# Optimization experiments

Hardware: AMD Instinct MI355X
Metric: run time of the kernel (lower is better)

The kernel has to match this reference:

```python
import jax, jax.numpy as jnp
import numpy as np

N, E = 25000, 400000
D_NODE, D_EDGE_IN, D_EH, D_H, D_DUAL = 128, 16, 128, 256, 128


def layer_norm(x, g, b, eps=1e-5):
    mu = jnp.mean(x, axis=-1, keepdims=True)
    var = jnp.mean((x - mu) ** 2, axis=-1, keepdims=True)
    return (x - mu) * jax.lax.rsqrt(var + eps) * g + b


def setup_inputs() -> dict:
    key = jax.random.key(0)
    ks = jax.random.split(key, 20)

    def w(k, shape):
        return (jax.random.normal(k, shape, dtype=jnp.float32) * 0.05)

    inp = {
        "node_embedding": jax.random.normal(ks[0], (N, D_NODE), dtype=jnp.float32),
        "edge_index": jax.random.randint(ks[1], (2, E), 0, N, dtype=jnp.int64),
        "edge_attr": jax.random.normal(ks[2], (E, D_EDGE_IN), dtype=jnp.float32),
        "dual_node_emb": jax.random.normal(ks[3], (E, D_DUAL), dtype=jnp.float32),
        "atom_reactivity_logits": jax.random.normal(ks[4], (N,), dtype=jnp.float32),
        "W_be1": w(ks[5], (D_EDGE_IN, D_EH)), "b_be1": jnp.zeros((D_EH,), jnp.float32),
        "g_be1": jnp.ones((D_EH,), jnp.float32), "bb_be1": jnp.zeros((D_EH,), jnp.float32),
        "W_be2": w(ks[6], (D_EH, D_EH)), "b_be2": jnp.zeros((D_EH,), jnp.float32),
        "g_be2": jnp.ones((D_EH,), jnp.float32), "bb_be2": jnp.zeros((D_EH,), jnp.float32),
        "W_be3": w(ks[7], (D_EH, D_EH)), "b_be3": jnp.zeros((D_EH,), jnp.float32),
        "g_be3": jnp.ones((D_EH,), jnp.float32), "bb_be3": jnp.zeros((D_EH,), jnp.float32),
        # DualGraphBondReactivityPredictor
        "W_d1": w(ks[8], (D_DUAL, D_H)), "b_d1": jnp.zeros((D_H,), jnp.float32),
        "W_d2": w(ks[9], (D_H, D_H)), "b_d2": jnp.zeros((D_H,), jnp.float32),
        "W_do": w(ks[10], (D_H, 1)), "b_do": jnp.zeros((1,), jnp.float32),
        # main head: in = 2*D_NODE + D_EH + 3 = 387
        "W_f1": w(ks[11], (2 * D_NODE + D_EH + 3, D_H)), "b_f1": jnp.zeros((D_H,), jnp.float32),
        "W_f2": w(ks[12], (D_H, D_H)), "b_f2": jnp.zeros((D_H,), jnp.float32),
        "W_bo": w(ks[13], (D_H, 1)), "b_bo": jnp.zeros((1,), jnp.float32),
    }
    return inp


def reference(node_embedding, edge_index, edge_attr, dual_node_emb, atom_reactivity_logits,
              W_be1, b_be1, g_be1, bb_be1, W_be2, b_be2, g_be2, bb_be2,
              W_be3, b_be3, g_be3, bb_be3,
              W_d1, b_d1, W_d2, b_d2, W_do, b_do,
              W_f1, b_f1, W_f2, b_f2, W_bo, b_bo):
    src, dst = edge_index[0], edge_index[1]

    # BondEmbedding (dropout = identity in eval mode)
    e = jax.nn.silu(layer_norm(edge_attr @ W_be1 + b_be1, g_be1, bb_be1))
    e = jax.nn.silu(layer_norm(e @ W_be2 + b_be2, g_be2, bb_be2))
    e = jax.nn.silu(layer_norm(e @ W_be3 + b_be3, g_be3, bb_be3))  # [E, D_EH]

    atom_p = jax.nn.sigmoid(atom_reactivity_logits)  # [N]
    p_src = atom_p[src][:, None]  # [E,1]
    p_dst = atom_p[dst][:, None]

    # dual-graph bond reactivity
    d = jax.nn.silu(dual_node_emb @ W_d1 + b_d1)
    d = jax.nn.silu(d @ W_d2 + b_d2)
    dual_p = jax.nn.sigmoid((d @ W_do + b_do)[:, 0])[:, None]  # [E,1]

    feats = jnp.concatenate(
        [node_embedding[src], node_embedding[dst], e, dual_p, p_src, p_dst], axis=-1
    )  # [E, 2*D_NODE + D_EH + 3]

    x = jax.nn.silu(feats @ W_f1 + b_f1)
    x = jax.nn.silu(x @ W_f2 + b_f2)
    return (x @ W_bo + b_bo)[:, 0]  # [E]
```

## Files before the change

kernel.cpp:

```cpp
#include <hip/hip_runtime.h>
#include <hip/hip_bf16.h>
#include <stdint.h>

typedef __attribute__((ext_vector_type(8))) short bf16x8;
typedef __attribute__((ext_vector_type(4))) float f32x4;
typedef __attribute__((ext_vector_type(4))) float float4v;

__device__ __forceinline__ uint16_t bfc(float x){
    __hip_bfloat16 h = __float2bfloat16(x);
    return __builtin_bit_cast(uint16_t, h);
}
__device__ __forceinline__ uint32_t pk2(float a, float b){
    return (uint32_t)bfc(a) | ((uint32_t)bfc(b) << 16);
}
__device__ __forceinline__ float fsigmoid(float x){ return 1.0f / (1.0f + __expf(-x)); }
__device__ __forceinline__ float fsilu(float x){ return x * fsigmoid(x); }

__device__ __forceinline__ bf16x8 pack8(float4v lo, float4v hi){
    bf16x8 r;
    r[0]=(short)bfc(lo[0]); r[1]=(short)bfc(lo[1]);
    r[2]=(short)bfc(lo[2]); r[3]=(short)bfc(lo[3]);
    r[4]=(short)bfc(hi[0]); r[5]=(short)bfc(hi[1]);
    r[6]=(short)bfc(hi[2]); r[7]=(short)bfc(hi[3]);
    return r;
}

#define SZ_BE1 4096
#define SZ_128 16384
#define SZ_D1  32768
#define SZ_D2  65536
#define SZ_F1  98304
#define OFF_BE1 0
#define OFF_BE2 (OFF_BE1 + SZ_BE1)
#define OFF_BE3 (OFF_BE2 + SZ_128)
#define OFF_D1  (OFF_BE3 + SZ_128)
#define OFF_D2  (OFF_D1 + SZ_D1)
#define OFF_F1  (OFF_D2 + SZ_D2)
#define OFF_F2  (OFF_F1 + SZ_F1)
#define WS_ELEMS (OFF_F2 + SZ_D2)

__device__ __forceinline__ int fragpos(int k, int c, int OUT){
    int kt = k >> 5, ct = c >> 4;
    int fid = kt * (OUT >> 4) + ct;
    int ln = ((k & 31) >> 3) * 16 + (c & 15);
    return fid * 512 + ln * 8 + (k & 7);
}

__global__ void __launch_bounds__(256)
prep_w(const float* __restrict__ Wbe1, const float* __restrict__ Wbe2,
       const float* __restrict__ Wbe3, const float* __restrict__ Wd1,
       const float* __restrict__ Wd2,  const float* __restrict__ Wf1,
       const float* __restrict__ Wf2,  uint16_t* __restrict__ ws){
    int t = blockIdx.x * 256 + threadIdx.x;
    if (t >= WS_ELEMS) return;
    if (t < OFF_BE2) {
        int u = t;            int k = u >> 7, c = u & 127;
        float v = (k < 16) ? Wbe1[k * 128 + c] : 0.0f;
        ws[OFF_BE1 + fragpos(k, c, 128)] = bfc(v);
    } else if (t < OFF_BE3) {
        int u = t - OFF_BE2;  int k = u >> 7, c = u & 127;
        ws[OFF_BE2 + fragpos(k, c, 128)] = bfc(Wbe2[u]);
    } else if (t < OFF_D1) {
        int u = t - OFF_BE3;  int k = u >> 7, c = u & 127;
        ws[OFF_BE3 + fragpos(k, c, 128)] = bfc(Wbe3[u]);
    } else if (t < OFF_D2) {
        int u = t - OFF_D1;   int k = u >> 8, c = u & 255;
        ws[OFF_D1 + fragpos(k, c, 256)] = bfc(Wd1[u]);
    } else if (t < OFF_F1) {
        int u = t - OFF_D2;   int k = u >> 8, c = u & 255;
        ws[OFF_D2 + fragpos(k, c, 256)] = bfc(Wd2[u]);
    } else if (t < OFF_F2) {
        int u = t - OFF_F1;   int k = u >> 8, c = u & 255;
        ws[OFF_F1 + fragpos(k, c, 256)] = bfc(Wf1[u]);
    } else {
        int u = t - OFF_F2;   int k = u >> 8, c = u & 255;
        ws[OFF_F2 + fragpos(k, c, 256)] = bfc(Wf2[u]);
    }
}

__global__ void __launch_bounds__(256)
prep_n(const float* __restrict__ src, uint16_t* __restrict__ dst, int n){
    int t = blockIdx.x * 256 + threadIdx.x;
    if (t < n) dst[t] = bfc(src[t]);
}

typedef const __attribute__((address_space(1))) void gas_void;
typedef __attribute__((address_space(3))) void las_void;
__device__ __forceinline__ void g2l16(const void* g, void* l){
    __builtin_amdgcn_global_load_lds((gas_void*)g, (las_void*)l, 16, 0, 0);
}

#define LDS_TOTAL 135168

__global__ void __launch_bounds__(512) __attribute__((amdgpu_waves_per_eu(2, 2)))
bond_fast_kernel(const int* __restrict__ edge_index,
                 const float* __restrict__ edge_attr, const float* __restrict__ dual_emb,
                 const float* __restrict__ logits,
                 const float* __restrict__ b_be1, const float* __restrict__ g_be1, const float* __restrict__ bb_be1,
                 const float* __restrict__ b_be2, const float* __restrict__ g_be2, const float* __restrict__ bb_be2,
                 const float* __restrict__ b_be3, const float* __restrict__ g_be3, const float* __restrict__ bb_be3,
                 const float* __restrict__ b_d1, const float* __restrict__ b_d2,
                 const float* __restrict__ W_do, const float* __restrict__ b_do,
                 const float* __restrict__ W_f1, const float* __restrict__ b_f1,
                 const float* __restrict__ b_f2,
                 const float* __restrict__ W_bo, const float* __restrict__ b_bo,
                 const uint16_t* __restrict__ ws, float* __restrict__ out, int E)
{
    __shared__ char lds[LDS_TOTAL];
    const int t    = threadIdx.x;
    const int wave = t >> 6;
    const int lane = t & 63;
    const int li   = lane & 15, lg = lane >> 4;
    const int eg   = wave >> 1;
    const int ch   = wave & 1;
    const int e0b  = blockIdx.x * 128;

    char* bufE = lds;
    char* h256 = lds + 32768;
    uint16_t* wb0 = (uint16_t*)(lds + 98304);
    uint16_t* wb1 = (uint16_t*)(lds + 114688);
    float* ps  = (float*)(lds + 131072);
    float* pd  = (float*)(lds + 131584);
    int* sidx  = (int*)(lds + 132096);
    int* didx  = (int*)(lds + 132608);
    float* dpp = (float*)(lds + 133120);
    float* bop = (float*)(lds + 134144);

    const uint8_t*  wsb = (const uint8_t*)ws;
    const uint16_t* nbf = ws + WS_ELEMS;

    if (t < 128) {
        int e = e0b + t; if (e >= E) e = E - 1;
        int s_ = edge_index[e];
        int d_ = edge_index[E + e];
        sidx[t] = s_; didx[t] = d_;
        ps[t] = fsigmoid(logits[s_]);
        pd[t] = fsigmoid(logits[d_]);
    }

    int cur = 0;
    auto stageW = [&](int elemoff, int big){
        uint8_t* dst = (uint8_t*)(cur ? wb0 : wb1) + t * 16;
        const uint8_t* g = wsb + (size_t)elemoff * 2 + t * 16;
        g2l16(g, dst);
        if (big) g2l16(g + 8192, dst + 8192);
    };
    auto stepend = [&](){ __syncthreads(); cur ^= 1; };
    auto curbuf  = [&]() -> const uint16_t* { return cur ? wb1 : wb0; };

    f32x4 acc[2][8];

    auto ldf = [&](const uint16_t* w, int fid) -> bf16x8 {
        return *(const bf16x8*)(w + fid * 512 + lane * 8);
    };
    auto grpBE = [&](const uint16_t* w, bf16x8 a0){
        #pragma unroll
        for (int ct = 0; ct < 8; ++ct){
            bf16x8 b = ldf(w, ct);
            acc[0][ct] = __builtin_amdgcn_mfma_f32_16x16x32_bf16(a0, b, acc[0][ct], 0, 0, 0);
        }
    };
    auto grp256 = [&](const uint16_t* w, bf16x8 a0, bf16x8 a1){
        #pragma unroll
        for (int ct = 0; ct < 8; ++ct){
            bf16x8 b = ldf(w, ch * 8 + ct);
            acc[0][ct] = __builtin_amdgcn_mfma_f32_16x16x32_bf16(a0, b, acc[0][ct], 0, 0, 0);
            acc[1][ct] = __builtin_amdgcn_mfma_f32_16x16x32_bf16(a1, b, acc[1][ct], 0, 0, 0);
        }
    };
    auto initBE = [&](const float* b){
        #pragma unroll
        for (int ct = 0; ct < 8; ++ct){
            float bv = b[li + 16 * ct];
            f32x4 iv = {bv, bv, bv, bv};
            acc[0][ct] = iv;
        }
    };
    auto init256 = [&](const float* b){
        #pragma unroll
        for (int ct = 0; ct < 8; ++ct){
            float bv = b[ch * 128 + ct * 16 + li];
            f32x4 iv = {bv, bv, bv, bv};
            acc[0][ct] = iv; acc[1][ct] = iv;
        }
    };
    auto eb_read = [&](int row, int kt) -> bf16x8 {
        int off = row * 256 + (kt * 32 + lg * 8) * 2;
        return *(const bf16x8*)(bufE + (off ^ ((row & 7) << 4)));
    };
    auto h2_read = [&](int row, int kt) -> bf16x8 {
        int off = row * 512 + (kt * 32 + lg * 8) * 2;
        return *(const bf16x8*)(h256 + (off ^ ((row & 7) << 4)));
    };
    auto lnstoreBE = [&](const float* g, const float* bb){
        #pragma unroll
        for (int r = 0; r < 4; ++r){
            float s = 0.f, q = 0.f;
            #pragma unroll
            for (int ct = 0; ct < 8; ++ct){ float v = acc[0][ct][r]; s += v; q += v*v; }
            s += __shfl_xor(s, 1); q += __shfl_xor(q, 1);
            s += __shfl_xor(s, 2); q += __shfl_xor(q, 2);
            s += __shfl_xor(s, 4); q += __shfl_xor(q, 4);
            s += __shfl_xor(s, 8); q += __shfl_xor(q, 8);
            float mu = s * 0.0078125f;
            float var = q * 0.0078125f - mu * mu;
            float rs = rsqrtf(var + 1e-5f);
            int row = wave * 16 + lg * 4 + r;
            int rswz = (row & 7) << 4;
            #pragma unroll
            for (int ct = 0; ct < 8; ++ct){
                int col = li + 16 * ct;
                float v = (acc[0][ct][r] - mu) * rs * g[col] + bb[col];
                int off = row * 256 + col * 2;
                *(uint16_t*)(bufE + (off ^ rswz)) = bfc(fsilu(v));
            }
        }
    };
    auto silustore256 = [&](){
        #pragma unroll
        for (int rt = 0; rt < 2; ++rt){
            #pragma unroll
            for (int r = 0; r < 4; ++r){
                int row = eg * 32 + rt * 16 + lg * 4 + r;
                int rswz = (row & 7) << 4;
                #pragma unroll
                for (int ct = 0; ct < 8; ++ct){
                    int off = row * 512 + (ch * 128 + ct * 16 + li) * 2;
                    *(uint16_t*)(h256 + (off ^ rswz)) = bfc(fsilu(acc[rt][ct][r]));
                }
            }
        }
    };

    {
        const uint8_t* g = wsb + t * 16;
        g2l16(g, (uint8_t*)wb0 + t * 16);
    }
    __syncthreads();

    {
        stageW(OFF_BE2, 0);
        bf16x8 aE = {0,0,0,0,0,0,0,0};
        if (lg < 2){
            int ea = e0b + wave * 16 + li; if (ea >= E) ea = E - 1;
            const float* pa = edge_attr + (size_t)ea * 16 + lg * 8;
            aE = pack8(*(const float4v*)pa, *(const float4v*)(pa + 4));
        }
        initBE(b_be1);
        grpBE(curbuf(), aE);
        lnstoreBE(g_be1, bb_be1);
        stepend();
    }

    initBE(b_be2);
    #pragma unroll 1
    for (int kt = 0; kt < 4; ++kt){
        if (kt < 3) stageW(OFF_BE2 + (kt + 1) * 4096, 0);
        else        stageW(OFF_BE3, 0);
        grpBE(curbuf(), eb_read(wave * 16 + li, kt));
        if (kt == 3) lnstoreBE(g_be2, bb_be2);
        stepend();
    }
    initBE(b_be3);
    #pragma unroll 1
    for (int kt = 0; kt < 4; ++kt){
        if (kt < 3) stageW(OFF_BE3 + (kt + 1) * 4096, 0);
        else        stageW(OFF_D1, 1);
        grpBE(curbuf(), eb_read(wave * 16 + li, kt));
        if (kt == 3) lnstoreBE(g_be3, bb_be3);
        stepend();
    }

    init256(b_d1);
    #pragma unroll 1
    for (int kt = 0; kt < 4; ++kt){
        float4v va0, va1, vb0, vb1;
        {
            int ea = e0b + eg * 32 + li;      if (ea >= E) ea = E - 1;
            int eb = e0b + eg * 32 + 16 + li; if (eb >= E) eb = E - 1;
            const float* pa = dual_emb + (size_t)ea * 128 + kt * 32 + lg * 8;
            const float* pb = dual_emb + (size_t)eb * 128 + kt * 32 + lg * 8;
            va0 = *(const float4v*)pa; va1 = *(const float4v*)(pa + 4);
            vb0 = *(const float4v*)pb; vb1 = *(const float4v*)(pb + 4);
        }
        if (kt < 3) stageW(OFF_D1 + (kt + 1) * 8192, 1);
        else        stageW(OFF_D2, 1);
        grp256(curbuf(), pack8(va0, va1), pack8(vb0, vb1));
        if (kt == 3) silustore256();
        stepend();
    }

    init256(b_d2);
    #pragma unroll 1
    for (int kt = 0; kt < 8; ++kt){
        if (kt < 7) stageW(OFF_D2 + (kt + 1) * 8192, 1);
        else        stageW(OFF_F1, 1);
        grp256(curbuf(), h2_read(eg * 32 + li, kt), h2_read(eg * 32 + 16 + li, kt));
        if (kt == 7){
            #pragma unroll
            for (int rt = 0; rt < 2; ++rt){
                #pragma unroll
                for (int r = 0; r < 4; ++r){
                    float s = 0.f;
                    #pragma unroll
                    for (int ct = 0; ct < 8; ++ct)
                        s += fsilu(acc[rt][ct][r]) * W_do[ch * 128 + ct * 16 + li];
                    s += __shfl_xor(s, 1); s += __shfl_xor(s, 2);
                    s += __shfl_xor(s, 4); s += __shfl_xor(s, 8);
                    if (li == 0) dpp[ch * 128 + eg * 32 + rt * 16 + lg * 4 + r] = s;
                }
            }
        }
        stepend();
    }

    {
        {
            float bdo0 = b_do[0];
            #pragma unroll
            for (int ct = 0; ct < 8; ++ct){
                int col = ch * 128 + ct * 16 + li;
                float bv = b_f1[col];
                float t0 = W_f1[384 * 256 + col];
                float t1 = W_f1[385 * 256 + col];
                float t2 = W_f1[386 * 256 + col];
                #pragma unroll
                for (int rt = 0; rt < 2; ++rt)
                    #pragma unroll
                    for (int r = 0; r < 4; ++r){
                        int row = eg * 32 + rt * 16 + lg * 4 + r;
                        float dv = fsigmoid(dpp[row] + dpp[128 + row] + bdo0);
                        acc[rt][ct][r] = bv + dv*t0 + ps[row]*t1 + pd[row]*t2;
                    }
            }
        }
        int s0 = sidx[eg * 32 + li],      s1 = sidx[eg * 32 + 16 + li];
        int d0 = didx[eg * 32 + li],      d1 = didx[eg * 32 + 16 + li];
        #pragma unroll 1
        for (int kt = 0; kt < 12; ++kt){
            bf16x8 a0, a1;
            if (kt < 8){
                int ra = (kt < 4) ? s0 : d0;
                int rb = (kt < 4) ? s1 : d1;
                int ko = (kt & 3) * 32 + lg * 8;
                a0 = *(const bf16x8*)(nbf + (size_t)ra * 128 + ko);
                a1 = *(const bf16x8*)(nbf + (size_t)rb * 128 + ko);
            } else {
                a0 = eb_read(eg * 32 + li, kt - 8);
                a1 = eb_read(eg * 32 + 16 + li, kt - 8);
            }
            if (kt < 11) stageW(OFF_F1 + (kt + 1) * 8192, 1);
            else         stageW(OFF_F2, 1);
            grp256(curbuf(), a0, a1);
            if (kt == 11) silustore256();
            stepend();
        }
    }

    init256(b_f2);
    #pragma unroll 1
    for (int kt = 0; kt < 8; ++kt){
        if (kt < 7) stageW(OFF_F2 + (kt + 1) * 8192, 1);
        grp256(curbuf(), h2_read(eg * 32 + li, kt), h2_read(eg * 32 + 16 + li, kt));
        if (kt == 7){
            #pragma unroll
            for (int rt = 0; rt < 2; ++rt){
                #pragma unroll
                for (int r = 0; r < 4; ++r){
                    float s = 0.f;
                    #pragma unroll
                    for (int ct = 0; ct < 8; ++ct)
                        s += fsilu(acc[rt][ct][r]) * W_bo[ch * 128 + ct * 16 + li];
                    s += __shfl_xor(s, 1); s += __shfl_xor(s, 2);
                    s += __shfl_xor(s, 4); s += __shfl_xor(s, 8);
                    if (li == 0) bop[ch * 128 + eg * 32 + rt * 16 + lg * 4 + r] = s;
                }
            }
        } else {
            stepend();
        }
    }
    __syncthreads();
    if (t < 128){
        int e = e0b + t;
        if (e < E) out[e] = bop[t] + bop[128 + t] + b_bo[0];
    }
}

__global__ void __launch_bounds__(512) __attribute__((amdgpu_waves_per_eu(2, 2)))
bond_fused_kernel(const float* __restrict__ node_emb, const int* __restrict__ edge_index,
                  const float* __restrict__ edge_attr, const float* __restrict__ dual_emb,
                  const float* __restrict__ logits,
                  const float* __restrict__ W_be1, const float* __restrict__ b_be1,
                  const float* __restrict__ g_be1, const float* __restrict__ bb_be1,
                  const float* __restrict__ W_be2, const float* __restrict__ b_be2,
                  const float* __restrict__ g_be2, const float* __restrict__ bb_be2,
                  const float* __restrict__ W_be3, const float* __restrict__ b_be3,
                  const float* __restrict__ g_be3, const float* __restrict__ bb_be3,
                  const float* __restrict__ W_d1, const float* __restrict__ b_d1,
                  const float* __restrict__ W_d2, const float* __restrict__ b_d2,
                  const float* __restrict__ W_do, const float* __restrict__ b_do,
                  const float* __restrict__ W_f1, const float* __restrict__ b_f1,
                  const float* __restrict__ W_f2, const float* __restrict__ b_f2,
                  const float* __restrict__ W_bo, const float* __restrict__ b_bo,
                  float* __restrict__ out, int E)
{
    __shared__ char lds[LDS_TOTAL];
    const int t    = threadIdx.x;
    const int wave = t >> 6;
    const int lane = t & 63;
    const int li   = lane & 15, lg = lane >> 4;
    const int eg   = wave >> 1;
    const int ch   = wave & 1;
    const int e0b  = blockIdx.x * 128;

    char* bufE = lds;
    char* h256 = lds + 32768;
    uint16_t* wb0 = (uint16_t*)(lds + 98304);
    uint16_t* wb1 = (uint16_t*)(lds + 114688);
    float* ps  = (float*)(lds + 131072);
    float* pd  = (float*)(lds + 131584);
    int* sidx  = (int*)(lds + 132096);
    int* didx  = (int*)(lds + 132608);
    float* dpp = (float*)(lds + 133120);
    float* bop = (float*)(lds + 134144);

    if (t < 128) {
        int e = e0b + t; if (e >= E) e = E - 1;
        int s_ = edge_index[e];
        int d_ = edge_index[E + e];
        sidx[t] = s_; didx[t] = d_;
        ps[t] = fsigmoid(logits[s_]);
        pd[t] = fsigmoid(logits[d_]);
    }

    float sr[2][8];
    auto issueW256 = [&](const float* W, int kbase){
        #pragma unroll
        for (int h = 0; h < 2; ++h){
            const float* p = W + (size_t)(kbase + lg * 8) * 256 + (wave + 8*h) * 16 + li;
            #pragma unroll
            for (int j = 0; j < 8; ++j) sr[h][j] = p[j * 256];
        }
    };
    auto issueW128 = [&](const float* W, int kbase, int K){
        const float* p = W + (size_t)(kbase + lg * 8) * 128 + wave * 16 + li;
        #pragma unroll
        for (int j = 0; j < 8; ++j)
            sr[0][j] = (kbase + lg * 8 + j < K) ? p[j * 128] : 0.f;
    };
    auto commitW = [&](uint16_t* dst, int nh){
        #pragma unroll
        for (int h = 0; h < 2; ++h){
            if (h < nh){
                uint4 w;
                w.x = pk2(sr[h][0], sr[h][1]); w.y = pk2(sr[h][2], sr[h][3]);
                w.z = pk2(sr[h][4], sr[h][5]); w.w = pk2(sr[h][6], sr[h][7]);
                *(uint4*)(dst + (wave + 8*h) * 512 + lane * 8) = w;
            }
        }
    };

    int cur = 0;
    auto stepend = [&](int mode){
        if (mode) commitW(cur ? wb0 : wb1, mode == 128 ? 1 : 2);
        __syncthreads();
        cur ^= 1;
    };
    auto curbuf = [&]() -> const uint16_t* { return cur ? wb1 : wb0; };

    f32x4 acc[2][8];

    auto ldf = [&](const uint16_t* w, int fid) -> bf16x8 {
        return *(const bf16x8*)(w + fid * 512 + lane * 8);
    };
    auto grpBE = [&](const uint16_t* w, bf16x8 a0){
        #pragma unroll
        for (int ct = 0; ct < 8; ++ct){
            bf16x8 b = ldf(w, ct);
            acc[0][ct] = __builtin_amdgcn_mfma_f32_16x16x32_bf16(a0, b, acc[0][ct], 0, 0, 0);
        }
    };
    auto grp256 = [&](const uint16_t* w, bf16x8 a0, bf16x8 a1){
        #pragma unroll
        for (int ct = 0; ct < 8; ++ct){
            bf16x8 b = ldf(w, ch * 8 + ct);
            acc[0][ct] = __builtin_amdgcn_mfma_f32_16x16x32_bf16(a0, b, acc[0][ct], 0, 0, 0);
            acc[1][ct] = __builtin_amdgcn_mfma_f32_16x16x32_bf16(a1, b, acc[1][ct], 0, 0, 0);
        }
    };
    auto initBE = [&](const float* b){
        #pragma unroll
        for (int ct = 0; ct < 8; ++ct){
            float bv = b[li + 16 * ct];
            f32x4 iv = {bv, bv, bv, bv};
            acc[0][ct] = iv;
        }
    };
    auto init256 = [&](const float* b){
        #pragma unroll
        for (int ct = 0; ct < 8; ++ct){
            float bv = b[ch * 128 + ct * 16 + li];
            f32x4 iv = {bv, bv, bv, bv};
            acc[0][ct] = iv; acc[1][ct] = iv;
        }
    };
    auto eb_read = [&](int row, int kt) -> bf16x8 {
        int off = row * 256 + (kt * 32 + lg * 8) * 2;
        return *(const bf16x8*)(bufE + (off ^ ((row & 7) << 4)));
    };
    auto h2_read = [&](int row, int kt) -> bf16x8 {
        int off = row * 512 + (kt * 32 + lg * 8) * 2;
        return *(const bf16x8*)(h256 + (off ^ ((row & 7) << 4)));
    };
    auto lnstoreBE = [&](const float* g, const float* bb){
        #pragma unroll
        for (int r = 0; r < 4; ++r){
            float s = 0.f, q = 0.f;
            #pragma unroll
            for (int ct = 0; ct < 8; ++ct){ float v = acc[0][ct][r]; s += v; q += v*v; }
            s += __shfl_xor(s, 1); q += __shfl_xor(q, 1);
            s += __shfl_xor(s, 2); q += __shfl_xor(q, 2);
            s += __shfl_xor(s, 4); q += __shfl_xor(q, 4);
            s += __shfl_xor(s, 8); q += __shfl_xor(q, 8);
            float mu = s * 0.0078125f;
            float var = q * 0.0078125f - mu * mu;
            float rs = rsqrtf(var + 1e-5f);
            int row = wave * 16 + lg * 4 + r;
            int rswz = (row & 7) << 4;
            #pragma unroll
            for (int ct = 0; ct < 8; ++ct){
                int col = li + 16 * ct;
                float v = (acc[0][ct][r] - mu) * rs * g[col] + bb[col];
                int off = row * 256 + col * 2;
                *(uint16_t*)(bufE + (off ^ rswz)) = bfc(fsilu(v));
            }
        }
    };
    auto silustore256 = [&](){
        #pragma unroll
        for (int rt = 0; rt < 2; ++rt){
            #pragma unroll
            for (int r = 0; r < 4; ++r){
                int row = eg * 32 + rt * 16 + lg * 4 + r;
                int rswz = (row & 7) << 4;
                #pragma unroll
                for (int ct = 0; ct < 8; ++ct){
                    int off = row * 512 + (ch * 128 + ct * 16 + li) * 2;
                    *(uint16_t*)(h256 + (off ^ rswz)) = bfc(fsilu(acc[rt][ct][r]));
                }
            }
        }
    };

    issueW128(W_be1, 0, 16);
    commitW(wb0, 1);
    __syncthreads();

    {
        bf16x8 aE = {0,0,0,0,0,0,0,0};
        if (lg < 2){
            int ea = e0b + wave * 16 + li; if (ea >= E) ea = E - 1;
            const float* pa = edge_attr + (size_t)ea * 16 + lg * 8;
            aE = pack8(*(const float4v*)pa, *(const float4v*)(pa + 4));
        }
        issueW128(W_be2, 0, 128);
        initBE(b_be1);
        grpBE(curbuf(), aE);
        lnstoreBE(g_be1, bb_be1);
        stepend(128);
    }

    initBE(b_be2);
    #pragma unroll 1
    for (int kt = 0; kt < 4; ++kt){
        if (kt < 3) issueW128(W_be2, (kt + 1) * 32, 128);
        else        issueW128(W_be3, 0, 128);
        grpBE(curbuf(), eb_read(wave * 16 + li, kt));
        if (kt == 3) lnstoreBE(g_be2, bb_be2);
        stepend(128);
    }
    initBE(b_be3);
    #pragma unroll 1
    for (int kt = 0; kt < 4; ++kt){
        if (kt < 3) issueW128(W_be3, (kt + 1) * 32, 128);
        else        issueW256(W_d1, 0);
        grpBE(curbuf(), eb_read(wave * 16 + li, kt));
        if (kt == 3) lnstoreBE(g_be3, bb_be3);
        stepend(kt < 3 ? 128 : 256);
    }

    init256(b_d1);
    #pragma unroll 1
    for (int kt = 0; kt < 4; ++kt){
        float4v va0, va1, vb0, vb1;
        {
            int ea = e0b + eg * 32 + li;      if (ea >= E) ea = E - 1;
            int eb = e0b + eg * 32 + 16 + li; if (eb >= E) eb = E - 1;
            const float* pa = dual_emb + (size_t)ea * 128 + kt * 32 + lg * 8;
            const float* pb = dual_emb + (size_t)eb * 128 + kt * 32 + lg * 8;
            va0 = *(const float4v*)pa; va1 = *(const float4v*)(pa + 4);
            vb0 = *(const float4v*)pb; vb1 = *(const float4v*)(pb + 4);
        }
        if (kt < 3) issueW256(W_d1, (kt + 1) * 32);
        else        issueW256(W_d2, 0);
        grp256(curbuf(), pack8(va0, va1), pack8(vb0, vb1));
        if (kt == 3) silustore256();
        stepend(256);
    }

    init256(b_d2);
    #pragma unroll 1
    for (int kt = 0; kt < 8; ++kt){
        if (kt < 7) issueW256(W_d2, (kt + 1) * 32);
        else        issueW256(W_f1, 0);
        grp256(curbuf(), h2_read(eg * 32 + li, kt), h2_read(eg * 32 + 16 + li, kt));
        if (kt == 7){
            #pragma unroll
            for (int rt = 0; rt < 2; ++rt){
                #pragma unroll
                for (int r = 0; r < 4; ++r){
                    float s = 0.f;
                    #pragma unroll
                    for (int ct = 0; ct < 8; ++ct)
                        s += fsilu(acc[rt][ct][r]) * W_do[ch * 128 + ct * 16 + li];
                    s += __shfl_xor(s, 1); s += __shfl_xor(s, 2);
                    s += __shfl_xor(s, 4); s += __shfl_xor(s, 8);
                    if (li == 0) dpp[ch * 128 + eg * 32 + rt * 16 + lg * 4 + r] = s;
                }
            }
        }
        stepend(256);
    }

    {
        {
            float bdo0 = b_do[0];
            #pragma unroll
            for (int ct = 0; ct < 8; ++ct){
                int col = ch * 128 + ct * 16 + li;
                float bv = b_f1[col];
                float t0 = W_f1[384 * 256 + col];
                float t1 = W_f1[385 * 256 + col];
                float t2 = W_f1[386 * 256 + col];
                #pragma unroll
                for (int rt = 0; rt < 2; ++rt)
                    #pragma unroll
                    for (int r = 0; r < 4; ++r){
                        int row = eg * 32 + rt * 16 + lg * 4 + r;
                        float dv = fsigmoid(dpp[row] + dpp[128 + row] + bdo0);
                        acc[rt][ct][r] = bv + dv*t0 + ps[row]*t1 + pd[row]*t2;
                    }
            }
        }
        int s0 = sidx[eg * 32 + li],      s1 = sidx[eg * 32 + 16 + li];
        int d0 = didx[eg * 32 + li],      d1 = didx[eg * 32 + 16 + li];
        #pragma unroll 1
        for (int kt = 0; kt < 12; ++kt){
            bf16x8 a0, a1;
            if (kt < 8){
                int ra = (kt < 4) ? s0 : d0;
                int rb = (kt < 4) ? s1 : d1;
                int ko = (kt & 3) * 32 + lg * 8;
                const float* pa = node_emb + (size_t)ra * 128 + ko;
                const float* pb = node_emb + (size_t)rb * 128 + ko;
                a0 = pack8(*(const float4v*)pa, *(const float4v*)(pa + 4));
                a1 = pack8(*(const float4v*)pb, *(const float4v*)(pb + 4));
            } else {
                a0 = eb_read(eg * 32 + li, kt - 8);
                a1 = eb_read(eg * 32 + 16 + li, kt - 8);
            }
            if (kt < 11) issueW256(W_f1, (kt + 1) * 32);
            else         issueW256(W_f2, 0);
            grp256(curbuf(), a0, a1);
            if (kt == 11) silustore256();
            stepend(256);
        }
    }

    init256(b_f2);
    #pragma unroll 1
    for (int kt = 0; kt < 8; ++kt){
        if (kt < 7) issueW256(W_f2, (kt + 1) * 32);
        grp256(curbuf(), h2_read(eg * 32 + li, kt), h2_read(eg * 32 + 16 + li, kt));
        if (kt == 7){
            #pragma unroll
            for (int rt = 0; rt < 2; ++rt){
                #pragma unroll
                for (int r = 0; r < 4; ++r){
                    float s = 0.f;
                    #pragma unroll
                    for (int ct = 0; ct < 8; ++ct)
                        s += fsilu(acc[rt][ct][r]) * W_bo[ch * 128 + ct * 16 + li];
                    s += __shfl_xor(s, 1); s += __shfl_xor(s, 2);
                    s += __shfl_xor(s, 4); s += __shfl_xor(s, 8);
                    if (li == 0) bop[ch * 128 + eg * 32 + rt * 16 + lg * 4 + r] = s;
                }
            }
        } else {
            stepend(256);
        }
    }
    __syncthreads();
    if (t < 128){
        int e = e0b + t;
        if (e < E) out[e] = bop[t] + bop[128 + t] + b_bo[0];
    }
}

extern "C" void kernel_launch(void* const* d_in, const int* in_sizes, int n_in,
                              void* d_out, int out_size, void* d_ws, size_t ws_size,
                              hipStream_t stream) {
    const float* node_emb   = (const float*)d_in[0];
    const int*   edge_index = (const int*)d_in[1];
    const float* edge_attr  = (const float*)d_in[2];
    const float* dual_emb   = (const float*)d_in[3];
    const float* logits     = (const float*)d_in[4];
    const float* W_be1 = (const float*)d_in[5];
    const float* b_be1 = (const float*)d_in[6];
    const float* g_be1 = (const float*)d_in[7];
    const float* bb_be1= (const float*)d_in[8];
    const float* W_be2 = (const float*)d_in[9];
    const float* b_be2 = (const float*)d_in[10];
    const float* g_be2 = (const float*)d_in[11];
    const float* bb_be2= (const float*)d_in[12];
    const float* W_be3 = (const float*)d_in[13];
    const float* b_be3 = (const float*)d_in[14];
    const float* g_be3 = (const float*)d_in[15];
    const float* bb_be3= (const float*)d_in[16];
    const float* W_d1  = (const float*)d_in[17];
    const float* b_d1  = (const float*)d_in[18];
    const float* W_d2  = (const float*)d_in[19];
    const float* b_d2  = (const float*)d_in[20];
    const float* W_do  = (const float*)d_in[21];
    const float* b_do  = (const float*)d_in[22];
    const float* W_f1  = (const float*)d_in[23];
    const float* b_f1  = (const float*)d_in[24];
    const float* W_f2  = (const float*)d_in[25];
    const float* b_f2  = (const float*)d_in[26];
    const float* W_bo  = (const float*)d_in[27];
    const float* b_bo  = (const float*)d_in[28];
    float* out = (float*)d_out;

    int E = in_sizes[2] / 16;
    int nblocks = (E + 127) / 128;
    size_t nodeElems = (size_t)in_sizes[0];
    size_t wsNeed = ((size_t)WS_ELEMS + nodeElems) * 2;

    if (ws_size >= wsNeed) {
        uint16_t* ws16 = (uint16_t*)d_ws;
        prep_w<<<dim3((WS_ELEMS + 255) / 256), dim3(256), 0, stream>>>(
            W_be1, W_be2, W_be3, W_d1, W_d2, W_f1, W_f2, ws16);
        prep_n<<<dim3((int)((nodeElems + 255) / 256)), dim3(256), 0, stream>>>(
            node_emb, ws16 + WS_ELEMS, (int)nodeElems);
        bond_fast_kernel<<<dim3(nblocks), dim3(512), 0, stream>>>(
            edge_index, edge_attr, dual_emb, logits,
            b_be1, g_be1, bb_be1,
            b_be2, g_be2, bb_be2,
            b_be3, g_be3, bb_be3,
            b_d1, b_d2, W_do, b_do,
            W_f1, b_f1, b_f2, W_bo, b_bo,
            ws16, out, E);
    } else {
        bond_fused_kernel<<<dim3(nblocks), dim3(512), 0, stream>>>(
            node_emb, edge_index, edge_attr, dual_emb, logits,
            W_be1, b_be1, g_be1, bb_be1,
            W_be2, b_be2, g_be2, bb_be2,
            W_be3, b_be3, g_be3, bb_be3,
            W_d1, b_d1, W_d2, b_d2, W_do, b_do,
            W_f1, b_f1, W_f2, b_f2, W_bo, b_bo,
            out, E);
    }
}
```

Measured before the change: 774.2 us.

## Double workgroup to 1024 threads, one 16-row tile per wave

The fast kernel now launches 1024 threads per 128-edge block instead of 512. Each wave handles a single 16-row M tile instead of two, so the accumulator array halves and register pressure drops. Weight staging is rebalanced: the upper 512 threads stage the 8 KB BondEmbedding slices while the lower 8 waves compute that stage, leaving half the waves idle during it. The goal is more waves in flight to hide latency, but each weight fragment read from LDS is now reused across only one A tile, which doubles LDS traffic per MFMA and adds more barrier participants.

New measurement: 805.5 us. 1.04x slower.

```diff
diff --git a/kernel.cpp b/kernel.cpp
--- a/kernel.cpp
+++ b/kernel.cpp
@@ -92,7 +92,7 @@
 
 #define LDS_TOTAL 135168
 
-__global__ void __launch_bounds__(512) __attribute__((amdgpu_waves_per_eu(2, 2)))
+__global__ void __launch_bounds__(1024) __attribute__((amdgpu_waves_per_eu(4, 4)))
 bond_fast_kernel(const int* __restrict__ edge_index,
                  const float* __restrict__ edge_attr, const float* __restrict__ dual_emb,
                  const float* __restrict__ logits,
@@ -139,16 +139,21 @@
     }
 
     int cur = 0;
-    auto stageW = [&](int elemoff, int big){
+    auto stageW16 = [&](int elemoff){
         uint8_t* dst = (uint8_t*)(cur ? wb0 : wb1) + t * 16;
-        const uint8_t* g = wsb + (size_t)elemoff * 2 + t * 16;
-        g2l16(g, dst);
-        if (big) g2l16(g + 8192, dst + 8192);
+        g2l16(wsb + (size_t)elemoff * 2 + t * 16, dst);
+    };
+    auto stageW8 = [&](int elemoff){
+        if (t >= 512){
+            int u = t - 512;
+            uint8_t* dst = (uint8_t*)(cur ? wb0 : wb1) + u * 16;
+            g2l16(wsb + (size_t)elemoff * 2 + u * 16, dst);
+        }
     };
     auto stepend = [&](){ __syncthreads(); cur ^= 1; };
     auto curbuf  = [&]() -> const uint16_t* { return cur ? wb1 : wb0; };
 
-    f32x4 acc[2][8];
+    f32x4 acc[8];
 
     auto ldf = [&](const uint16_t* w, int fid) -> bf16x8 {
         return *(const bf16x8*)(w + fid * 512 + lane * 8);
@@ -157,15 +162,14 @@
         #pragma unroll
         for (int ct = 0; ct < 8; ++ct){
             bf16x8 b = ldf(w, ct);
-            acc[0][ct] = __builtin_amdgcn_mfma_f32_16x16x32_bf16(a0, b, acc[0][ct], 0, 0, 0);
-        }
-    };
-    auto grp256 = [&](const uint16_t* w, bf16x8 a0, bf16x8 a1){
+            acc[ct] = __builtin_amdgcn_mfma_f32_16x16x32_bf16(a0, b, acc[ct], 0, 0, 0);
+        }
+    };
+    auto grp256 = [&](const uint16_t* w, bf16x8 a0){
         #pragma unroll
         for (int ct = 0; ct < 8; ++ct){
             bf16x8 b = ldf(w, ch * 8 + ct);
-            acc[0][ct] = __builtin_amdgcn_mfma_f32_16x16x32_bf16(a0, b, acc[0][ct], 0, 0, 0);
-            acc[1][ct] = __builtin_amdgcn_mfma_f32_16x16x32_bf16(a1, b, acc[1][ct], 0, 0, 0);
+            acc[ct] = __builtin_amdgcn_mfma_f32_16x16x32_bf16(a0, b, acc[ct], 0, 0, 0);
         }
     };
     auto initBE = [&](const float* b){
@@ -173,7 +177,7 @@
         for (int ct = 0; ct < 8; ++ct){
             float bv = b[li + 16 * ct];
             f32x4 iv = {bv, bv, bv, bv};
-            acc[0][ct] = iv;
+            acc[ct] = iv;
         }
     };
     auto init256 = [&](const float* b){
@@ -181,7 +185,7 @@
         for (int ct = 0; ct < 8; ++ct){
             float bv = b[ch * 128 + ct * 16 + li];
             f32x4 iv = {bv, bv, bv, bv};
-            acc[0][ct] = iv; acc[1][ct] = iv;
+            acc[ct] = iv;
         }
     };
     auto eb_read = [&](int row, int kt) -> bf16x8 {
@@ -197,7 +201,7 @@
         for (int r = 0; r < 4; ++r){
             float s = 0.f, q = 0.f;
             #pragma unroll
-            for (int ct = 0; ct < 8; ++ct){ float v = acc[0][ct][r]; s += v; q += v*v; }
+            for (int ct = 0; ct < 8; ++ct){ float v = acc[ct][r]; s += v; q += v*v; }
             s += __shfl_xor(s, 1); q += __shfl_xor(q, 1);
             s += __shfl_xor(s, 2); q += __shfl_xor(q, 2);
             s += __shfl_xor(s, 4); q += __shfl_xor(q, 4);
@@ -210,7 +214,7 @@
             #pragma unroll
             for (int ct = 0; ct < 8; ++ct){
                 int col = li + 16 * ct;
-                float v = (acc[0][ct][r] - mu) * rs * g[col] + bb[col];
+                float v = (acc[ct][r] - mu) * rs * g[col] + bb[col];
                 int off = row * 256 + col * 2;
                 *(uint16_t*)(bufE + (off ^ rswz)) = bfc(fsilu(v));
             }
@@ -218,74 +222,74 @@
     };
     auto silustore256 = [&](){
         #pragma unroll
-        for (int rt = 0; rt < 2; ++rt){
-            #pragma unroll
-            for (int r = 0; r < 4; ++r){
-                int row = eg * 32 + rt * 16 + lg * 4 + r;
-                int rswz = (row & 7) << 4;
-                #pragma unroll
-                for (int ct = 0; ct < 8; ++ct){
-                    int off = row * 512 + (ch * 128 + ct * 16 + li) * 2;
-                    *(uint16_t*)(h256 + (off ^ rswz)) = bfc(fsilu(acc[rt][ct][r]));
-                }
-            }
-        }
-    };
+        for (int r = 0; r < 4; ++r){
+            int row = eg * 16 + lg * 4 + r;
+            int rswz = (row & 7) << 4;
+            #pragma unroll
+            for (int ct = 0; ct < 8; ++ct){
+                int off = row * 512 + (ch * 128 + ct * 16 + li) * 2;
+                *(uint16_t*)(h256 + (off ^ rswz)) = bfc(fsilu(acc[ct][r]));
+            }
+        }
+    };
+
+    if (t >= 512){
+        int u = t - 512;
+        g2l16(wsb + u * 16, (uint8_t*)wb0 + u * 16);
+    }
+    __syncthreads();
 
     {
-        const uint8_t* g = wsb + t * 16;
-        g2l16(g, (uint8_t*)wb0 + t * 16);
-    }
-    __syncthreads();
-
-    {
-        stageW(OFF_BE2, 0);
-        bf16x8 aE = {0,0,0,0,0,0,0,0};
-        if (lg < 2){
-            int ea = e0b + wave * 16 + li; if (ea >= E) ea = E - 1;
-            const float* pa = edge_attr + (size_t)ea * 16 + lg * 8;
-            aE = pack8(*(const float4v*)pa, *(const float4v*)(pa + 4));
-        }
-        initBE(b_be1);
-        grpBE(curbuf(), aE);
-        lnstoreBE(g_be1, bb_be1);
+        stageW8(OFF_BE2);
+        if (wave < 8){
+            bf16x8 aE = {0,0,0,0,0,0,0,0};
+            if (lg < 2){
+                int ea = e0b + wave * 16 + li; if (ea >= E) ea = E - 1;
+                const float* pa = edge_attr + (size_t)ea * 16 + lg * 8;
+                aE = pack8(*(const float4v*)pa, *(const float4v*)(pa + 4));
+            }
+            initBE(b_be1);
+            grpBE(curbuf(), aE);
+            lnstoreBE(g_be1, bb_be1);
+        }
         stepend();
     }
 
-    initBE(b_be2);
+    if (wave < 8) initBE(b_be2);
     #pragma unroll 1
     for (int kt = 0; kt < 4; ++kt){
-        if (kt < 3) stageW(OFF_BE2 + (kt + 1) * 4096, 0);
-        else        stageW(OFF_BE3, 0);
-        grpBE(curbuf(), eb_read(wave * 16 + li, kt));
-        if (kt == 3) lnstoreBE(g_be2, bb_be2);
+        if (kt < 3) stageW8(OFF_BE2 + (kt + 1) * 4096);
+        else        stageW8(OFF_BE3);
+        if (wave < 8){
+            grpBE(curbuf(), eb_read(wave * 16 + li, kt));
+            if (kt == 3) lnstoreBE(g_be2, bb_be2);
+        }
         stepend();
     }
-    initBE(b_be3);
+    if (wave < 8) initBE(b_be3);
     #pragma unroll 1
     for (int kt = 0; kt < 4; ++kt){
-        if (kt < 3) stageW(OFF_BE3 + (kt + 1) * 4096, 0);
-        else        stageW(OFF_D1, 1);
-        grpBE(curbuf(), eb_read(wave * 16 + li, kt));
-        if (kt == 3) lnstoreBE(g_be3, bb_be3);
+        if (kt < 3) stageW8(OFF_BE3 + (kt + 1) * 4096);
+        else        stageW16(OFF_D1);
+        if (wave < 8){
+            grpBE(curbuf(), eb_read(wave * 16 + li, kt));
+            if (kt == 3) lnstoreBE(g_be3, bb_be3);
+        }
         stepend();
     }
 
     init256(b_d1);
     #pragma unroll 1
     for (int kt = 0; kt < 4; ++kt){
-        float4v va0, va1, vb0, vb1;
+        float4v va0, va1;
         {
-            int ea = e0b + eg * 32 + li;      if (ea >= E) ea = E - 1;
-            int eb = e0b + eg * 32 + 16 + li; if (eb >= E) eb = E - 1;
+            int ea = e0b + eg * 16 + li; if (ea >= E) ea = E - 1;
             const float* pa = dual_emb + (size_t)ea * 128 + kt * 32 + lg * 8;
-            const float* pb = dual_emb + (size_t)eb * 128 + kt * 32 + lg * 8;
             va0 = *(const float4v*)pa; va1 = *(const float4v*)(pa + 4);
-            vb0 = *(const float4v*)pb; vb1 = *(const float4v*)(pb + 4);
-        }
-        if (kt < 3) stageW(OFF_D1 + (kt + 1) * 8192, 1);
-        else        stageW(OFF_D2, 1);
-        grp256(curbuf(), pack8(va0, va1), pack8(vb0, vb1));
+        }
+        if (kt < 3) stageW16(OFF_D1 + (kt + 1) * 8192);
+        else        stageW16(OFF_D2);
+        grp256(curbuf(), pack8(va0, va1));
         if (kt == 3) silustore256();
         stepend();
     }
@@ -293,22 +297,19 @@
     init256(b_d2);
     #pragma unroll 1
     for (int kt = 0; kt < 8; ++kt){
-        if (kt < 7) stageW(OFF_D2 + (kt + 1) * 8192, 1);
-        else        stageW(OFF_F1, 1);
-        grp256(curbuf(), h2_read(eg * 32 + li, kt), h2_read(eg * 32 + 16 + li, kt));
+        if (kt < 7) stageW16(OFF_D2 + (kt + 1) * 8192);
+        else        stageW16(OFF_F1);
+        grp256(curbuf(), h2_read(eg * 16 + li, kt));
         if (kt == 7){
             #pragma unroll
-            for (int rt = 0; rt < 2; ++rt){
+            for (int r = 0; r < 4; ++r){
+                float s = 0.f;
                 #pragma unroll
-                for (int r = 0; r < 4; ++r){
-                    float s = 0.f;
-                    #pragma unroll
-                    for (int ct = 0; ct < 8; ++ct)
-                        s += fsilu(acc[rt][ct][r]) * W_do[ch * 128 + ct * 16 + li];
-                    s += __shfl_xor(s, 1); s += __shfl_xor(s, 2);
-                    s += __shfl_xor(s, 4); s += __shfl_xor(s, 8);
-                    if (li == 0) dpp[ch * 128 + eg * 32 + rt * 16 + lg * 4 + r] = s;
-                }
+                for (int ct = 0; ct < 8; ++ct)
+                    s += fsilu(acc[ct][r]) * W_do[ch * 128 + ct * 16 + li];
+                s += __shfl_xor(s, 1); s += __shfl_xor(s, 2);
+                s += __shfl_xor(s, 4); s += __shfl_xor(s, 8);
+                if (li == 0) dpp[ch * 128 + eg * 16 + lg * 4 + r] = s;
             }
         }
         stepend();
@@ -317,6 +318,13 @@
     {
         {
             float bdo0 = b_do[0];
+            float dvv[4], psr[4], pdr[4];
+            #pragma unroll
+            for (int r = 0; r < 4; ++r){
+                int row = eg * 16 + lg * 4 + r;
+                dvv[r] = fsigmoid(dpp[row] + dpp[128 + row] + bdo0);
+                psr[r] = ps[row]; pdr[r] = pd[row];
+            }
             #pragma unroll
             for (int ct = 0; ct < 8; ++ct){
                 int col = ch * 128 + ct * 16 + li;
@@ -325,33 +333,25 @@
                 float t1 = W_f1[385 * 256 + col];
                 float t2 = W_f1[386 * 256 + col];
                 #pragma unroll
-                for (int rt = 0; rt < 2; ++rt)
-                    #pragma unroll
-                    for (int r = 0; r < 4; ++r){
-                        int row = eg * 32 + rt * 16 + lg * 4 + r;
-                        float dv = fsigmoid(dpp[row] + dpp[128 + row] + bdo0);
-                        acc[rt][ct][r] = bv + dv*t0 + ps[row]*t1 + pd[row]*t2;
-                    }
-            }
-        }
-        int s0 = sidx[eg * 32 + li],      s1 = sidx[eg * 32 + 16 + li];
-        int d0 = didx[eg * 32 + li],      d1 = didx[eg * 32 + 16 + li];
+                for (int r = 0; r < 4; ++r)
+                    acc[ct][r] = bv + dvv[r]*t0 + psr[r]*t1 + pdr[r]*t2;
+            }
+        }
+        int s0 = sidx[eg * 16 + li];
+        int d0 = didx[eg * 16 + li];
         #pragma unroll 1
         for (int kt = 0; kt < 12; ++kt){
-            bf16x8 a0, a1;
+            bf16x8 a0;
             if (kt < 8){
                 int ra = (kt < 4) ? s0 : d0;
-                int rb = (kt < 4) ? s1 : d1;
                 int ko = (kt & 3) * 32 + lg * 8;
                 a0 = *(const bf16x8*)(nbf + (size_t)ra * 128 + ko);
-                a1 = *(const bf16x8*)(nbf + (size_t)rb * 128 + ko);
             } else {
-                a0 = eb_read(eg * 32 + li, kt - 8);
-                a1 = eb_read(eg * 32 + 16 + li, kt - 8);
-            }
-            if (kt < 11) stageW(OFF_F1 + (kt + 1) * 8192, 1);
-            else         stageW(OFF_F2, 1);
-            grp256(curbuf(), a0, a1);
+                a0 = eb_read(eg * 16 + li, kt - 8);
+            }
+            if (kt < 11) stageW16(OFF_F1 + (kt + 1) * 8192);
+            else         stageW16(OFF_F2);
+            grp256(curbuf(), a0);
             if (kt == 11) silustore256();
             stepend();
         }
@@ -360,21 +360,18 @@
     init256(b_f2);
     #pragma unroll 1
     for (int kt = 0; kt < 8; ++kt){
-        if (kt < 7) stageW(OFF_F2 + (kt + 1) * 8192, 1);
-        grp256(curbuf(), h2_read(eg * 32 + li, kt), h2_read(eg * 32 + 16 + li, kt));
+        if (kt < 7) stageW16(OFF_F2 + (kt + 1) * 8192);
+        grp256(curbuf(), h2_read(eg * 16 + li, kt));
         if (kt == 7){
             #pragma unroll
-            for (int rt = 0; rt < 2; ++rt){
+            for (int r = 0; r < 4; ++r){
+                float s = 0.f;
                 #pragma unroll
-                for (int r = 0; r < 4; ++r){
-                    float s = 0.f;
-                    #pragma unroll
-                    for (int ct = 0; ct < 8; ++ct)
-                        s += fsilu(acc[rt][ct][r]) * W_bo[ch * 128 + ct * 16 + li];
-                    s += __shfl_xor(s, 1); s += __shfl_xor(s, 2);
-                    s += __shfl_xor(s, 4); s += __shfl_xor(s, 8);
-                    if (li == 0) bop[ch * 128 + eg * 32 + rt * 16 + lg * 4 + r] = s;
-                }
+                for (int ct = 0; ct < 8; ++ct)
+                    s += fsilu(acc[ct][r]) * W_bo[ch * 128 + ct * 16 + li];
+                s += __shfl_xor(s, 1); s += __shfl_xor(s, 2);
+                s += __shfl_xor(s, 4); s += __shfl_xor(s, 8);
+                if (li == 0) bop[ch * 128 + eg * 16 + lg * 4 + r] = s;
             }
         } else {
             stepend();
@@ -387,6 +384,7 @@
     }
 }
 
+#define LDS_TOTAL_FB 135168
 __global__ void __launch_bounds__(512) __attribute__((amdgpu_waves_per_eu(2, 2)))
 bond_fused_kernel(const float* __restrict__ node_emb, const int* __restrict__ edge_index,
                   const float* __restrict__ edge_attr, const float* __restrict__ dual_emb,
@@ -405,7 +403,7 @@
                   const float* __restrict__ W_bo, const float* __restrict__ b_bo,
                   float* __restrict__ out, int E)
 {
-    __shared__ char lds[LDS_TOTAL];
+    __shared__ char lds[LDS_TOTAL_FB];
     const int t    = threadIdx.x;
     const int wave = t >> 6;
     const int lane = t & 63;
@@ -753,7 +751,7 @@
             W_be1, W_be2, W_be3, W_d1, W_d2, W_f1, W_f2, ws16);
         prep_n<<<dim3((int)((nodeElems + 255) / 256)), dim3(256), 0, stream>>>(
             node_emb, ws16 + WS_ELEMS, (int)nodeElems);
-        bond_fast_kernel<<<dim3(nblocks), dim3(512), 0, stream>>>(
+        bond_fast_kernel<<<dim3(nblocks), dim3(1024), 0, stream>>>(
             edge_index, edge_attr, dual_emb, logits,
             b_be1, g_be1, bb_be1,
             b_be2, g_be2, bb_be2,
```
